# Kernel tuning notes

Measured on AMD Instinct MI355X. Metric: run time of the kernel, lower is better.

## Reference

```python
import jax, jax.numpy as jnp
import numpy as np

NUM_GRAPHS = 500
BN_EPS = 1e-5


def setup_inputs() -> dict:
    key = jax.random.key(0)
    ks = jax.random.split(key, 16)
    N, E, F, D, L = 100000, 1600000, 128, 128, 3
    x = jax.random.normal(ks[0], (N, F), dtype=jnp.float32)
    edge_index = jax.random.randint(ks[1], (2, E), 0, N)
    batch = jnp.sort(jax.random.randint(ks[2], (N,), 0, NUM_GRAPHS))
    s = 1.0 / np.sqrt(F)
    sd = 1.0 / np.sqrt(D)
    # SAGEConv layer 0: out = lin_l(mean_aggr(x_j)) + lin_r(x)
    sage_Wl = jax.random.uniform(ks[3], (F, D), jnp.float32, -s, s)
    sage_bl = jax.random.uniform(ks[4], (D,), jnp.float32, -s, s)
    sage_Wr = jax.random.uniform(ks[5], (F, D), jnp.float32, -s, s)
    # GINConv layers 1..L-1: nn = Linear(D,D) -> ReLU -> Linear(D,D)
    gin_W1 = jax.random.uniform(ks[6], (L - 1, D, D), jnp.float32, -sd, sd)
    gin_b1 = jax.random.uniform(ks[7], (L - 1, D), jnp.float32, -sd, sd)
    gin_W2 = jax.random.uniform(ks[8], (L - 1, D, D), jnp.float32, -sd, sd)
    gin_b2 = jax.random.uniform(ks[9], (L - 1, D), jnp.float32, -sd, sd)
    bn_gamma = jnp.ones((L, D), dtype=jnp.float32)
    bn_beta = jnp.zeros((L, D), dtype=jnp.float32)
    return {"x": x, "edge_index": edge_index, "batch": batch,
            "sage_Wl": sage_Wl, "sage_bl": sage_bl, "sage_Wr": sage_Wr,
            "gin_W1": gin_W1, "gin_b1": gin_b1, "gin_W2": gin_W2, "gin_b2": gin_b2,
            "bn_gamma": bn_gamma, "bn_beta": bn_beta}


def _batchnorm(h, gamma, beta):
    mu = jnp.mean(h, axis=0)
    var = jnp.var(h, axis=0)  # biased, as torch BN uses for normalization
    return (h - mu) * jax.lax.rsqrt(var + BN_EPS) * gamma + beta


def reference(x, edge_index, batch, sage_Wl, sage_bl, sage_Wr,
              gin_W1, gin_b1, gin_W2, gin_b2, bn_gamma, bn_beta):
    N = x.shape[0]
    src, dst = edge_index[0], edge_index[1]
    L = bn_gamma.shape[0]

    # Layer 0: SAGEConv (mean aggregation, root weight, no bias on lin_r)
    deg = jax.ops.segment_sum(jnp.ones_like(dst, dtype=x.dtype), dst, num_segments=N)
    aggr = jax.ops.segment_sum(x[src], dst, num_segments=N)
    aggr = aggr / jnp.maximum(deg, 1.0)[:, None]
    h = aggr @ sage_Wl + sage_bl + x @ sage_Wr
    h = jax.nn.relu(h)
    h = _batchnorm(h, bn_gamma[0], bn_beta[0])
    xs = [h]

    # Layers 1..L-1: GINConv (eps=0): nn(x + sum_aggr(x_j))
    for i in range(1, L):
        aggr = jax.ops.segment_sum(h[src], dst, num_segments=N)
        t = h + aggr
        t = jax.nn.relu(t @ gin_W1[i - 1] + gin_b1[i - 1])
        t = t @ gin_W2[i - 1] + gin_b2[i - 1]
        h = jax.nn.relu(t)
        h = _batchnorm(h, bn_gamma[i], bn_beta[i])
        xs.append(h)

    # pooling != 'last': concat global_add_pool over every layer
    pooled = jnp.concatenate(
        [jax.ops.segment_sum(xi, batch, num_segments=NUM_GRAPHS) for xi in xs], axis=1)
    node_feats = jnp.concatenate(xs, axis=1)
    return (pooled, node_feats)
```

## Files before the change

kernel.cpp:

```cpp
#include <hip/hip_runtime.h>
#include <hip/hip_bf16.h>


#define BN_EPS 1e-5f
#define EPB 4096

typedef short s8v __attribute__((ext_vector_type(8)));
typedef float f4v __attribute__((ext_vector_type(4)));

__device__ __forceinline__ float bflo(unsigned u) { return __uint_as_float(u << 16); }
__device__ __forceinline__ float bfhi(unsigned u) { return __uint_as_float(u & 0xffff0000u); }
__device__ __forceinline__ unsigned short f2bf(float f) {
    unsigned u = __float_as_uint(f);
    unsigned r = (u + 0x7fffu + ((u >> 16) & 1u)) >> 16;
    return (unsigned short)r;
}
__device__ __forceinline__ unsigned pk2(float a, float b) {
    return (unsigned)f2bf(a) | ((unsigned)f2bf(b) << 16);
}
__device__ __forceinline__ void unpack8(uint4 u, float* v) {
    v[0] = bflo(u.x); v[1] = bfhi(u.x);
    v[2] = bflo(u.y); v[3] = bfhi(u.y);
    v[4] = bflo(u.z); v[5] = bfhi(u.z);
    v[6] = bflo(u.w); v[7] = bfhi(u.w);
}


__global__ __launch_bounds__(256) void k_binA(const int* __restrict__ src,
                                              const int* __restrict__ dst, int E, int NB, int CAP,
                                              int* __restrict__ bcnt,
                                              unsigned long long* __restrict__ ebuf) {
    __shared__ int hist[512], base[512], cur[512];
    const int tid = threadIdx.x;
    const int e0 = blockIdx.x * EPB;
    for (int i = tid; i < 512; i += 256) { hist[i] = 0; cur[i] = 0; }
    __syncthreads();
#pragma unroll
    for (int k = 0; k < EPB / 256; k++) {
        int e = e0 + k * 256 + tid;
        if (e < E) atomicAdd(&hist[dst[e] >> 8], 1);
    }
    __syncthreads();
    for (int b = tid; b < NB; b += 256)
        base[b] = hist[b] ? atomicAdd(&bcnt[b], hist[b]) : 0;
    __syncthreads();
#pragma unroll
    for (int k = 0; k < EPB / 256; k++) {
        int e = e0 + k * 256 + tid;
        if (e < E) {
            int d = dst[e];
            int b = d >> 8;
            int lp = atomicAdd(&cur[b], 1);
            int gp = base[b] + lp;
            if (gp < CAP)
                ebuf[(size_t)b * CAP + gp] = ((unsigned long long)d << 32) | (unsigned)src[e];
        }
    }
}

__global__ void k_bscan(const int* __restrict__ bcnt, int NB, int* __restrict__ bbase) {
    __shared__ int sm[256];
    const int tid = threadIdx.x;
    const int c = (NB + 255) / 256;
    int s = 0;
    for (int k = 0; k < c; k++) { int i = tid * c + k; if (i < NB) s += bcnt[i]; }
    sm[tid] = s;
    __syncthreads();
    for (int off = 1; off < 256; off <<= 1) {
        int v = (tid >= off) ? sm[tid - off] : 0;
        __syncthreads();
        sm[tid] += v;
        __syncthreads();
    }
    int run = sm[tid] - s;
    for (int k = 0; k < c; k++) {
        int i = tid * c + k;
        if (i < NB) { bbase[i] = run; run += bcnt[i]; }
    }
}

__global__ __launch_bounds__(256) void k_binB(const unsigned long long* __restrict__ ebuf,
                                              int CAP, const int* __restrict__ bcnt,
                                              const int* __restrict__ bbase,
                                              int N, int E,
                                              int* __restrict__ rp, int* __restrict__ csr) {
    __shared__ int deg[256], sc[256], cur[256];
    const int tid = threadIdx.x;
    const int b = blockIdx.x;
    const int cnt = min(bcnt[b], CAP);
    const int cbase = bbase[b];
    deg[tid] = 0;
    __syncthreads();
    const unsigned long long* eb = ebuf + (size_t)b * CAP;
    for (int i = tid; i < cnt; i += 256) {
        int d = (int)(eb[i] >> 32);
        atomicAdd(&deg[d & 255], 1);
    }
    __syncthreads();
    int myDeg = deg[tid];
    sc[tid] = myDeg;
    __syncthreads();
    for (int off = 1; off < 256; off <<= 1) {
        int v = (tid >= off) ? sc[tid - off] : 0;
        __syncthreads();
        sc[tid] += v;
        __syncthreads();
    }
    int pos = cbase + sc[tid] - myDeg;
    int node = b * 256 + tid;
    if (node < N) rp[node] = pos;
    cur[tid] = pos;
    __syncthreads();
    for (int i = tid; i < cnt; i += 256) {
        unsigned long long e = eb[i];
        int d = (int)(e >> 32);
        int p = atomicAdd(&cur[d & 255], 1);
        csr[p] = (int)(e & 0xffffffffu);
    }
    if (b == 0 && tid == 0) rp[N] = E;
}


__global__ void k_cvt_bf16(const float* __restrict__ in, uint4* __restrict__ out, int n8) {
    int i = blockIdx.x * 256 + threadIdx.x;
    if (i >= n8) return;
    const float4* p = reinterpret_cast<const float4*>(in) + (size_t)i * 2;
    float4 a = p[0], b = p[1];
    uint4 o;
    o.x = pk2(a.x, a.y); o.y = pk2(a.z, a.w);
    o.z = pk2(b.x, b.y); o.w = pk2(b.z, b.w);
    out[i] = o;
}

__global__ void k_pack_w(const float* __restrict__ W, unsigned short* __restrict__ out) {
    int idx = blockIdx.x * 256 + threadIdx.x;
    int k = idx >> 7, d = idx & 127;
    float w = W[idx];
    unsigned short h = f2bf(w);
    float hf = __uint_as_float((unsigned)h << 16);
    unsigned short l = f2bf(w - hf);
    int o = (((k >> 3) * 128) + d) * 8 + (k & 7);
    out[o] = h;
    out[16384 + o] = l;
}


template <bool SELF, bool MEAN>
__global__ void k_aggr(const int* __restrict__ rp, const int* __restrict__ csr,
                       const uint4* __restrict__ src, uint4* __restrict__ out, int N) {
    int node = blockIdx.x * 16 + (threadIdx.x >> 4);
    if (node >= N) return;
    int c = threadIdx.x & 15;
    float acc[8];
    if (SELF) {
        unpack8(src[(size_t)node * 16 + c], acc);
    } else {
#pragma unroll
        for (int k = 0; k < 8; k++) acc[k] = 0.f;
    }
    int lo = rp[node], hi = rp[node + 1];
    for (int j = lo; j < hi; j++) {
        int sn = csr[j];
        float v[8];
        unpack8(src[(size_t)sn * 16 + c], v);
#pragma unroll
        for (int k = 0; k < 8; k++) acc[k] += v[k];
    }
    if (MEAN) {
        float inv = 1.0f / fmaxf((float)(hi - lo), 1.0f);
#pragma unroll
        for (int k = 0; k < 8; k++) acc[k] *= inv;
    }
    uint4 o;
    o.x = pk2(acc[0], acc[1]); o.y = pk2(acc[2], acc[3]);
    o.z = pk2(acc[4], acc[5]); o.w = pk2(acc[6], acc[7]);
    out[(size_t)node * 16 + c] = o;
}


template <int TERMS, bool F32OUT, bool STATS>
__global__ __launch_bounds__(256) void k_gemm_mfma(
    const uint4* __restrict__ A1, const uint4* __restrict__ A2,
    const uint4* __restrict__ Wfrag,
    const float* __restrict__ bias,
    float* __restrict__ outF,
    unsigned short* __restrict__ outB,
    float* __restrict__ gsum, float* __restrict__ gsq,
    int N) {
    __shared__ float sred[4][128][2];
    const int tid = threadIdx.x;
    const int lane = tid & 63, wid = tid >> 6;
    const int nbase = blockIdx.x * 128 + wid * 32;
    const int l16 = lane & 15, lg = lane >> 4;

    f4v acc[2][8];
#pragma unroll
    for (int nf = 0; nf < 2; nf++)
#pragma unroll
        for (int df = 0; df < 8; df++) {
            acc[nf][df][0] = 0.f; acc[nf][df][1] = 0.f;
            acc[nf][df][2] = 0.f; acc[nf][df][3] = 0.f;
        }

#pragma unroll
    for (int t = 0; t < TERMS; t++) {
        const uint4* A = t ? A2 : A1;
        const uint4* Whi = Wfrag + (size_t)t * 4096;
        const uint4* Wlo = Whi + 2048;
        uint4 bvec[2][4];
#pragma unroll
        for (int nf = 0; nf < 2; nf++) {
            const uint4* row = A + (size_t)(nbase + nf * 16 + l16) * 16;
#pragma unroll
            for (int ks = 0; ks < 4; ks++) bvec[nf][ks] = row[ks * 4 + lg];
        }
#pragma unroll
        for (int ks = 0; ks < 4; ks++) {
            s8v b0 = __builtin_bit_cast(s8v, bvec[0][ks]);
            s8v b1 = __builtin_bit_cast(s8v, bvec[1][ks]);
#pragma unroll
            for (int df = 0; df < 8; df++) {
                int wi = (ks * 4 + lg) * 128 + df * 16 + l16;
                s8v ah = __builtin_bit_cast(s8v, Whi[wi]);
                s8v al = __builtin_bit_cast(s8v, Wlo[wi]);
                acc[0][df] = __builtin_amdgcn_mfma_f32_16x16x32_bf16(ah, b0, acc[0][df], 0, 0, 0);
                acc[1][df] = __builtin_amdgcn_mfma_f32_16x16x32_bf16(ah, b1, acc[1][df], 0, 0, 0);
                acc[0][df] = __builtin_amdgcn_mfma_f32_16x16x32_bf16(al, b0, acc[0][df], 0, 0, 0);
                acc[1][df] = __builtin_amdgcn_mfma_f32_16x16x32_bf16(al, b1, acc[1][df], 0, 0, 0);
            }
        }
    }

    const bool v0 = (nbase + 0 * 16 + l16) < N;
    const bool v1 = (nbase + 1 * 16 + l16) < N;
    float4 oo[2][8];
#pragma unroll
    for (int df = 0; df < 8; df++) {
        int d0 = df * 16 + lg * 4;
        const float4 bb = *reinterpret_cast<const float4*>(bias + d0);
#pragma unroll
        for (int nf = 0; nf < 2; nf++) {
            oo[nf][df].x = fmaxf(acc[nf][df][0] + bb.x, 0.f);
            oo[nf][df].y = fmaxf(acc[nf][df][1] + bb.y, 0.f);
            oo[nf][df].z = fmaxf(acc[nf][df][2] + bb.z, 0.f);
            oo[nf][df].w = fmaxf(acc[nf][df][3] + bb.w, 0.f);
        }
    }

    if (STATS) {
#pragma unroll
        for (int df = 0; df < 8; df++) {
            float s[4], q[4];
#pragma unroll
            for (int r = 0; r < 4; r++) {
                float a0 = v0 ? (&oo[0][df].x)[r] : 0.f;
                float a1 = v1 ? (&oo[1][df].x)[r] : 0.f;
                s[r] = a0 + a1;
                q[r] = a0 * a0 + a1 * a1;
            }
#pragma unroll
            for (int m = 1; m < 16; m <<= 1) {
#pragma unroll
                for (int r = 0; r < 4; r++) {
                    s[r] += __shfl_xor(s[r], m, 64);
                    q[r] += __shfl_xor(q[r], m, 64);
                }
            }
            if (l16 == 0) {
#pragma unroll
                for (int r = 0; r < 4; r++) {
                    sred[wid][df * 16 + lg * 4 + r][0] = s[r];
                    sred[wid][df * 16 + lg * 4 + r][1] = q[r];
                }
            }
        }
        __syncthreads();
        if (tid < 128) {
            float s = sred[0][tid][0] + sred[1][tid][0] + sred[2][tid][0] + sred[3][tid][0];
            float q = sred[0][tid][1] + sred[1][tid][1] + sred[2][tid][1] + sred[3][tid][1];
            unsafeAtomicAdd(&gsum[tid], s);
            unsafeAtomicAdd(&gsq[tid], q);
        }
    }

#pragma unroll
    for (int nf = 0; nf < 2; nf++) {
        int n = nbase + nf * 16 + l16;
        if (n < N) {
#pragma unroll
            for (int df = 0; df < 8; df++) {
                int d0 = df * 16 + lg * 4;
                if (F32OUT) {
                    *reinterpret_cast<float4*>(outF + (size_t)n * 384 + d0) = oo[nf][df];
                } else {
                    uint2 p;
                    p.x = pk2(oo[nf][df].x, oo[nf][df].y);
                    p.y = pk2(oo[nf][df].z, oo[nf][df].w);
                    *reinterpret_cast<uint2*>(outB + (size_t)n * 128 + d0) = p;
                }
            }
        }
    }
}


__global__ void k_bnfin(const float* __restrict__ gsum, const float* __restrict__ gsq,
                        const float* __restrict__ gamma, const float* __restrict__ beta,
                        int N, float* __restrict__ a, float* __restrict__ c) {
    int d = threadIdx.x;
    float invN = 1.0f / (float)N;
    float mu = gsum[d] * invN;
    float var = gsq[d] * invN - mu * mu;
    float rs = rsqrtf(var + BN_EPS);
    float aa = gamma[d] * rs;
    a[d] = aa;
    c[d] = beta[d] - mu * aa;
}

template <bool BF16IN>
__global__ void k_norm2(const void* __restrict__ in, int ldin,
                        const float* __restrict__ sa, const float* __restrict__ sc,
                        float* __restrict__ outF, uint4* __restrict__ outB, int N) {
    int idx = blockIdx.x * 256 + threadIdx.x;
    if (idx >= N * 16) return;
    int n = idx >> 4, cc = idx & 15;
    float v[8];
    if (BF16IN) {
        unpack8(reinterpret_cast<const uint4*>(in)[(size_t)n * 16 + cc], v);
    } else {
        const float* p = (const float*)in + (size_t)n * ldin + cc * 8;
        float4 x0 = *reinterpret_cast<const float4*>(p);
        float4 x1 = *reinterpret_cast<const float4*>(p + 4);
        v[0] = x0.x; v[1] = x0.y; v[2] = x0.z; v[3] = x0.w;
        v[4] = x1.x; v[5] = x1.y; v[6] = x1.z; v[7] = x1.w;
    }
    const float4 a0 = *reinterpret_cast<const float4*>(sa + cc * 8);
    const float4 a1 = *reinterpret_cast<const float4*>(sa + cc * 8 + 4);
    const float4 c0 = *reinterpret_cast<const float4*>(sc + cc * 8);
    const float4 c1 = *reinterpret_cast<const float4*>(sc + cc * 8 + 4);
    float y[8];
    y[0] = fmaf(v[0], a0.x, c0.x); y[1] = fmaf(v[1], a0.y, c0.y);
    y[2] = fmaf(v[2], a0.z, c0.z); y[3] = fmaf(v[3], a0.w, c0.w);
    y[4] = fmaf(v[4], a1.x, c1.x); y[5] = fmaf(v[5], a1.y, c1.y);
    y[6] = fmaf(v[6], a1.z, c1.z); y[7] = fmaf(v[7], a1.w, c1.w);
    float* po = outF + (size_t)n * 384 + cc * 8;
    *reinterpret_cast<float4*>(po) = make_float4(y[0], y[1], y[2], y[3]);
    *reinterpret_cast<float4*>(po + 4) = make_float4(y[4], y[5], y[6], y[7]);
    if (outB) {
        uint4 o;
        o.x = pk2(y[0], y[1]); o.y = pk2(y[2], y[3]);
        o.z = pk2(y[4], y[5]); o.w = pk2(y[6], y[7]);
        outB[(size_t)n * 16 + cc] = o;
    }
}


__device__ __forceinline__ int lbound(const int* __restrict__ b, int n, int v) {
    int lo = 0, hi = n;
    while (lo < hi) {
        int m = (lo + hi) >> 1;
        if (b[m] < v) lo = m + 1; else hi = m;
    }
    return lo;
}

__global__ void k_pool(const float* __restrict__ nf, const int* __restrict__ batch,
                       int N, float* __restrict__ out) {
    int g = blockIdx.x;
    int d = threadIdx.x;
    int lo = lbound(batch, N, g);
    int hi = lbound(batch, N, g + 1);
    float s = 0.f;
    for (int n = lo; n < hi; n++) s += nf[(size_t)n * 384 + d];
    out[(size_t)g * 384 + d] = s;
}


extern "C" void kernel_launch(void* const* d_in, const int* in_sizes, int n_in,
                              void* d_out, int out_size, void* d_ws, size_t ws_size,
                              hipStream_t stream) {
    const float* x   = (const float*)d_in[0];
    const int*   ei  = (const int*)d_in[1];
    const int*   bat = (const int*)d_in[2];
    const float* sWl = (const float*)d_in[3];
    const float* sbl = (const float*)d_in[4];
    const float* sWr = (const float*)d_in[5];
    const float* gW1 = (const float*)d_in[6];
    const float* gb1 = (const float*)d_in[7];
    const float* gW2 = (const float*)d_in[8];
    const float* gb2 = (const float*)d_in[9];
    const float* bng = (const float*)d_in[10];
    const float* bnb = (const float*)d_in[11];

    const int N = in_sizes[0] / 128;
    const int E = in_sizes[1] / 2;
    const int G = out_size / 384 - N;
    const int* srcp = ei;
    const int* dstp = ei + E;

    char* w = (char*)d_ws;
    auto alloc = [&](size_t bytes) -> void* {
        void* p = (void*)w;
        w += (bytes + 255) & ~(size_t)255;
        return p;
    };
    const size_t Npad = (size_t)(N + 128);
    int*   rp    = (int*)alloc(((size_t)N + 1) * 4);
    int*   csr   = (int*)alloc((size_t)E * 4);
    int*   bcnt  = (int*)alloc(8192);
    int*   bbase = (int*)alloc(8192);
    float* gsum  = (float*)alloc(512);
    float* gsq   = (float*)alloc(512);
    float* abuf  = (float*)alloc(512);
    float* cbuf  = (float*)alloc(512);
    unsigned short* Wp = (unsigned short*)alloc((size_t)6 * 2 * 16384 * 2);
    unsigned short* ab = (unsigned short*)alloc(Npad * 256);
    unsigned short* tb = (unsigned short*)alloc(Npad * 256);

    float* pooled = (float*)d_out;
    float* nf     = pooled + (size_t)G * 384;

    const int NB  = (N + 255) / 256;
    int CAP = ((2 * (E / (NB > 0 ? NB : 1)) + 511) / 512) * 512;
    const long long maxcap = (long long)(Npad * 256) / ((long long)NB * 8);
    if ((long long)CAP > maxcap) CAP = (int)(maxcap & ~511LL);
    unsigned long long* ebuf = (unsigned long long*)ab;

    const int egrid = (E + EPB - 1) / EPB;
    const int agrid = (N + 15) / 16;
    const int ggrid = (N + 127) / 128;
    const int vgrid = (N * 16 + 255) / 256;

    hipMemsetAsync(bcnt, 0, (size_t)NB * 4, stream);
    k_binA<<<egrid, 256, 0, stream>>>(srcp, dstp, E, NB, CAP, bcnt, ebuf);
    k_bscan<<<1, 256, 0, stream>>>(bcnt, NB, bbase);
    k_binB<<<NB, 256, 0, stream>>>(ebuf, CAP, bcnt, bbase, N, E, rp, csr);

    k_cvt_bf16<<<vgrid, 256, 0, stream>>>(x, (uint4*)tb, N * 16);
    k_pack_w<<<64, 256, 0, stream>>>(sWl,         Wp + 0 * 32768);
    k_pack_w<<<64, 256, 0, stream>>>(sWr,         Wp + 1 * 32768);
    k_pack_w<<<64, 256, 0, stream>>>(gW1,         Wp + 2 * 32768);
    k_pack_w<<<64, 256, 0, stream>>>(gW2,         Wp + 3 * 32768);
    k_pack_w<<<64, 256, 0, stream>>>(gW1 + 16384, Wp + 4 * 32768);
    k_pack_w<<<64, 256, 0, stream>>>(gW2 + 16384, Wp + 5 * 32768);

    k_aggr<false, true><<<agrid, 256, 0, stream>>>(rp, csr, (const uint4*)tb, (uint4*)ab, N);
    hipMemsetAsync(gsum, 0, 1024, stream);
    k_gemm_mfma<2, true, true><<<ggrid, 256, 0, stream>>>(
        (const uint4*)ab, (const uint4*)tb, (const uint4*)Wp, sbl, nf, nullptr,
        gsum, gsq, N);
    k_bnfin<<<1, 128, 0, stream>>>(gsum, gsq, bng, bnb, N, abuf, cbuf);
    k_norm2<false><<<vgrid, 256, 0, stream>>>(nf, 384, abuf, cbuf, nf, (uint4*)tb, N);

    for (int l = 1; l < 3; l++) {
        const uint4* W1p = (const uint4*)(Wp + (size_t)(2 + (l - 1) * 2) * 32768);
        const uint4* W2p = (const uint4*)(Wp + (size_t)(3 + (l - 1) * 2) * 32768);
        const float* b1 = gb1 + (size_t)(l - 1) * 128;
        const float* b2 = gb2 + (size_t)(l - 1) * 128;
        float* nfl = nf + (size_t)l * 128;

        k_aggr<true, false><<<agrid, 256, 0, stream>>>(rp, csr, (const uint4*)tb, (uint4*)ab, N);
        k_gemm_mfma<1, false, false><<<ggrid, 256, 0, stream>>>(
            (const uint4*)ab, nullptr, W1p, b1, nullptr, tb, nullptr, nullptr, N);
        hipMemsetAsync(gsum, 0, 1024, stream);
        k_gemm_mfma<1, true, true><<<ggrid, 256, 0, stream>>>(
            (const uint4*)tb, nullptr, W2p, b2, nfl, nullptr, gsum, gsq, N);
        k_bnfin<<<1, 128, 0, stream>>>(gsum, gsq, bng + l * 128, bnb + l * 128, N, abuf, cbuf);
        k_norm2<false><<<vgrid, 256, 0, stream>>>(nfl, 384, abuf, cbuf, nfl,
                                                  (l < 2) ? (uint4*)tb : nullptr, N);
    }

    k_pool<<<G, 384, 0, stream>>>(nf, bat, N, pooled);
}
```

Before: 669.8 us.

## Fuse GIN MLP GEMMs via LDS and defer BN normalization into pooling

The two GIN linear layers now run in one kernel: the ReLU'd hidden tile is staged as bf16 in swizzled shared memory rather than written to and re-read from global memory. Per-layer batchnorm is no longer written back to the fp32 output right away. Only the bf16 copy needed by the next layer is normalized, and one final kernel applies all three layers' scale/shift in place while accumulating graph pooling with atomics. Memsets are folded into bnfin. This removes several full passes over the N×384 output and the intermediate buffer, at the cost of atomics in pooling and higher shared-memory use per GEMM block.

```diff
diff --git a/kernel.cpp b/kernel.cpp
--- a/kernel.cpp
+++ b/kernel.cpp
@@ -144,6 +144,27 @@
     out[16384 + o] = l;
 }
 
+__global__ void k_cvt_h(const float* __restrict__ y,
+                        const float* __restrict__ sa, const float* __restrict__ sc,
+                        uint4* __restrict__ out, int N) {
+    int idx = blockIdx.x * 256 + threadIdx.x;
+    if (idx >= N * 16) return;
+    int n = idx >> 4, cc = idx & 15;
+    const float* p = y + (size_t)n * 384 + cc * 8;
+    float4 x0 = *reinterpret_cast<const float4*>(p);
+    float4 x1 = *reinterpret_cast<const float4*>(p + 4);
+    const float4 a0 = *reinterpret_cast<const float4*>(sa + cc * 8);
+    const float4 a1 = *reinterpret_cast<const float4*>(sa + cc * 8 + 4);
+    const float4 c0 = *reinterpret_cast<const float4*>(sc + cc * 8);
+    const float4 c1 = *reinterpret_cast<const float4*>(sc + cc * 8 + 4);
+    uint4 o;
+    o.x = pk2(fmaf(x0.x, a0.x, c0.x), fmaf(x0.y, a0.y, c0.y));
+    o.y = pk2(fmaf(x0.z, a0.z, c0.z), fmaf(x0.w, a0.w, c0.w));
+    o.z = pk2(fmaf(x1.x, a1.x, c1.x), fmaf(x1.y, a1.y, c1.y));
+    o.w = pk2(fmaf(x1.z, a1.z, c1.z), fmaf(x1.w, a1.w, c1.w));
+    out[(size_t)n * 16 + cc] = o;
+}
+
 
 template <bool SELF, bool MEAN>
 __global__ void k_aggr(const int* __restrict__ rp, const int* __restrict__ csr,
@@ -178,14 +199,66 @@
 }
 
 
-template <int TERMS, bool F32OUT, bool STATS>
-__global__ __launch_bounds__(256) void k_gemm_mfma(
+#define MFMA_STAGE(Whi, Wlo, B0, B1, ACC)                                          \
+    _Pragma("unroll")                                                              \
+    for (int ks = 0; ks < 4; ks++) {                                               \
+        s8v b0 = __builtin_bit_cast(s8v, B0[ks]);                                  \
+        s8v b1 = __builtin_bit_cast(s8v, B1[ks]);                                  \
+        _Pragma("unroll")                                                          \
+        for (int df = 0; df < 8; df++) {                                           \
+            int wi = (ks * 4 + lg) * 128 + df * 16 + l16;                          \
+            s8v ah = __builtin_bit_cast(s8v, Whi[wi]);                             \
+            s8v al = __builtin_bit_cast(s8v, Wlo[wi]);                             \
+            ACC[0][df] = __builtin_amdgcn_mfma_f32_16x16x32_bf16(ah, b0, ACC[0][df], 0, 0, 0); \
+            ACC[1][df] = __builtin_amdgcn_mfma_f32_16x16x32_bf16(ah, b1, ACC[1][df], 0, 0, 0); \
+            ACC[0][df] = __builtin_amdgcn_mfma_f32_16x16x32_bf16(al, b0, ACC[0][df], 0, 0, 0); \
+            ACC[1][df] = __builtin_amdgcn_mfma_f32_16x16x32_bf16(al, b1, ACC[1][df], 0, 0, 0); \
+        }                                                                          \
+    }
+
+#define STATS_EPILOGUE(OO, V0, V1)                                                 \
+    {                                                                              \
+        _Pragma("unroll")                                                          \
+        for (int df = 0; df < 8; df++) {                                           \
+            float s[4], q[4];                                                      \
+            _Pragma("unroll")                                                      \
+            for (int r = 0; r < 4; r++) {                                          \
+                float a0 = V0 ? (&OO[0][df].x)[r] : 0.f;                           \
+                float a1 = V1 ? (&OO[1][df].x)[r] : 0.f;                           \
+                s[r] = a0 + a1;                                                    \
+                q[r] = a0 * a0 + a1 * a1;                                          \
+            }                                                                      \
+            _Pragma("unroll")                                                      \
+            for (int m = 1; m < 16; m <<= 1) {                                     \
+                _Pragma("unroll")                                                  \
+                for (int r = 0; r < 4; r++) {                                      \
+                    s[r] += __shfl_xor(s[r], m, 64);                               \
+                    q[r] += __shfl_xor(q[r], m, 64);                               \
+                }                                                                  \
+            }                                                                      \
+            if (l16 == 0) {                                                        \
+                _Pragma("unroll")                                                  \
+                for (int r = 0; r < 4; r++) {                                      \
+                    sred[wid][df * 16 + lg * 4 + r][0] = s[r];                     \
+                    sred[wid][df * 16 + lg * 4 + r][1] = q[r];                     \
+                }                                                                  \
+            }                                                                      \
+        }                                                                          \
+        __syncthreads();                                                           \
+        if (tid < 128) {                                                           \
+            float s = sred[0][tid][0] + sred[1][tid][0] + sred[2][tid][0] + sred[3][tid][0]; \
+            float q = sred[0][tid][1] + sred[1][tid][1] + sred[2][tid][1] + sred[3][tid][1]; \
+            unsafeAtomicAdd(&gsum[tid], s);                                        \
+            unsafeAtomicAdd(&gsq[tid], q);                                         \
+        }                                                                          \
+    }
+
+
+__global__ __launch_bounds__(256) void k_gemm_sage(
     const uint4* __restrict__ A1, const uint4* __restrict__ A2,
     const uint4* __restrict__ Wfrag,
     const float* __restrict__ bias,
-    float* __restrict__ outF,
-    unsigned short* __restrict__ outB,
-    float* __restrict__ gsum, float* __restrict__ gsq,
+    float* __restrict__ outF, float* __restrict__ gsum, float* __restrict__ gsq,
     int N) {
     __shared__ float sred[4][128][2];
     const int tid = threadIdx.x;
@@ -197,13 +270,11 @@
 #pragma unroll
     for (int nf = 0; nf < 2; nf++)
 #pragma unroll
-        for (int df = 0; df < 8; df++) {
-            acc[nf][df][0] = 0.f; acc[nf][df][1] = 0.f;
-            acc[nf][df][2] = 0.f; acc[nf][df][3] = 0.f;
-        }
-
-#pragma unroll
-    for (int t = 0; t < TERMS; t++) {
+        for (int df = 0; df < 8; df++)
+            acc[nf][df] = (f4v){0.f, 0.f, 0.f, 0.f};
+
+#pragma unroll
+    for (int t = 0; t < 2; t++) {
         const uint4* A = t ? A2 : A1;
         const uint4* Whi = Wfrag + (size_t)t * 4096;
         const uint4* Wlo = Whi + 2048;
@@ -214,25 +285,11 @@
 #pragma unroll
             for (int ks = 0; ks < 4; ks++) bvec[nf][ks] = row[ks * 4 + lg];
         }
-#pragma unroll
-        for (int ks = 0; ks < 4; ks++) {
-            s8v b0 = __builtin_bit_cast(s8v, bvec[0][ks]);
-            s8v b1 = __builtin_bit_cast(s8v, bvec[1][ks]);
-#pragma unroll
-            for (int df = 0; df < 8; df++) {
-                int wi = (ks * 4 + lg) * 128 + df * 16 + l16;
-                s8v ah = __builtin_bit_cast(s8v, Whi[wi]);
-                s8v al = __builtin_bit_cast(s8v, Wlo[wi]);
-                acc[0][df] = __builtin_amdgcn_mfma_f32_16x16x32_bf16(ah, b0, acc[0][df], 0, 0, 0);
-                acc[1][df] = __builtin_amdgcn_mfma_f32_16x16x32_bf16(ah, b1, acc[1][df], 0, 0, 0);
-                acc[0][df] = __builtin_amdgcn_mfma_f32_16x16x32_bf16(al, b0, acc[0][df], 0, 0, 0);
-                acc[1][df] = __builtin_amdgcn_mfma_f32_16x16x32_bf16(al, b1, acc[1][df], 0, 0, 0);
-            }
-        }
-    }
-
-    const bool v0 = (nbase + 0 * 16 + l16) < N;
-    const bool v1 = (nbase + 1 * 16 + l16) < N;
+        MFMA_STAGE(Whi, Wlo, bvec[0], bvec[1], acc)
+    }
+
+    const bool v0 = (nbase + l16) < N;
+    const bool v1 = (nbase + 16 + l16) < N;
     float4 oo[2][8];
 #pragma unroll
     for (int df = 0; df < 8; df++) {
@@ -247,64 +304,124 @@
         }
     }
 
-    if (STATS) {
-#pragma unroll
-        for (int df = 0; df < 8; df++) {
-            float s[4], q[4];
-#pragma unroll
-            for (int r = 0; r < 4; r++) {
-                float a0 = v0 ? (&oo[0][df].x)[r] : 0.f;
-                float a1 = v1 ? (&oo[1][df].x)[r] : 0.f;
-                s[r] = a0 + a1;
-                q[r] = a0 * a0 + a1 * a1;
-            }
-#pragma unroll
-            for (int m = 1; m < 16; m <<= 1) {
-#pragma unroll
-                for (int r = 0; r < 4; r++) {
-                    s[r] += __shfl_xor(s[r], m, 64);
-                    q[r] += __shfl_xor(q[r], m, 64);
-                }
-            }
-            if (l16 == 0) {
-#pragma unroll
-                for (int r = 0; r < 4; r++) {
-                    sred[wid][df * 16 + lg * 4 + r][0] = s[r];
-                    sred[wid][df * 16 + lg * 4 + r][1] = q[r];
-                }
-            }
-        }
-        __syncthreads();
-        if (tid < 128) {
-            float s = sred[0][tid][0] + sred[1][tid][0] + sred[2][tid][0] + sred[3][tid][0];
-            float q = sred[0][tid][1] + sred[1][tid][1] + sred[2][tid][1] + sred[3][tid][1];
-            unsafeAtomicAdd(&gsum[tid], s);
-            unsafeAtomicAdd(&gsq[tid], q);
-        }
-    }
+    STATS_EPILOGUE(oo, v0, v1)
 
 #pragma unroll
     for (int nf = 0; nf < 2; nf++) {
         int n = nbase + nf * 16 + l16;
         if (n < N) {
 #pragma unroll
-            for (int df = 0; df < 8; df++) {
-                int d0 = df * 16 + lg * 4;
-                if (F32OUT) {
-                    *reinterpret_cast<float4*>(outF + (size_t)n * 384 + d0) = oo[nf][df];
-                } else {
-                    uint2 p;
-                    p.x = pk2(oo[nf][df].x, oo[nf][df].y);
-                    p.y = pk2(oo[nf][df].z, oo[nf][df].w);
-                    *reinterpret_cast<uint2*>(outB + (size_t)n * 128 + d0) = p;
-                }
-            }
-        }
-    }
-}
-
-
-__global__ void k_bnfin(const float* __restrict__ gsum, const float* __restrict__ gsq,
+            for (int df = 0; df < 8; df++)
+                *reinterpret_cast<float4*>(outF + (size_t)n * 384 + df * 16 + lg * 4) = oo[nf][df];
+        }
+    }
+}
+
+
+__global__ __launch_bounds__(256) void k_gemm_gin(
+    const uint4* __restrict__ A,
+    const uint4* __restrict__ W1f, const uint4* __restrict__ W2f,
+    const float* __restrict__ b1, const float* __restrict__ b2,
+    float* __restrict__ outF, float* __restrict__ gsum, float* __restrict__ gsq,
+    int N) {
+    __shared__ uint4 tile[2048];
+    __shared__ float sred[4][128][2];
+    const int tid = threadIdx.x;
+    const int lane = tid & 63, wid = tid >> 6;
+    const int nbase = blockIdx.x * 128 + wid * 32;
+    const int l16 = lane & 15, lg = lane >> 4;
+
+    f4v acc[2][8];
+#pragma unroll
+    for (int nf = 0; nf < 2; nf++)
+#pragma unroll
+        for (int df = 0; df < 8; df++)
+            acc[nf][df] = (f4v){0.f, 0.f, 0.f, 0.f};
+
+    {
+        const uint4* Whi = W1f;
+        const uint4* Wlo = W1f + 2048;
+        uint4 bvec[2][4];
+#pragma unroll
+        for (int nf = 0; nf < 2; nf++) {
+            const uint4* row = A + (size_t)(nbase + nf * 16 + l16) * 16;
+#pragma unroll
+            for (int ks = 0; ks < 4; ks++) bvec[nf][ks] = row[ks * 4 + lg];
+        }
+        MFMA_STAGE(Whi, Wlo, bvec[0], bvec[1], acc)
+    }
+#pragma unroll
+    for (int df = 0; df < 8; df++) {
+        int d0 = df * 16 + lg * 4;
+        const float4 bb = *reinterpret_cast<const float4*>(b1 + d0);
+#pragma unroll
+        for (int nf = 0; nf < 2; nf++) {
+            float tx = fmaxf(acc[nf][df][0] + bb.x, 0.f);
+            float ty = fmaxf(acc[nf][df][1] + bb.y, 0.f);
+            float tz = fmaxf(acc[nf][df][2] + bb.z, 0.f);
+            float tw = fmaxf(acc[nf][df][3] + bb.w, 0.f);
+            uint2 p;
+            p.x = pk2(tx, ty);
+            p.y = pk2(tz, tw);
+            int row = wid * 32 + nf * 16 + l16;
+            int col4 = df * 2 + (lg >> 1);
+            int slot = row * 16 + (col4 ^ (row & 15));
+            *reinterpret_cast<uint2*>(
+                reinterpret_cast<char*>(tile) + (size_t)slot * 16 + (lg & 1) * 8) = p;
+        }
+    }
+    __syncthreads();
+
+#pragma unroll
+    for (int nf = 0; nf < 2; nf++)
+#pragma unroll
+        for (int df = 0; df < 8; df++)
+            acc[nf][df] = (f4v){0.f, 0.f, 0.f, 0.f};
+    {
+        const uint4* Whi = W2f;
+        const uint4* Wlo = W2f + 2048;
+        uint4 bvec[2][4];
+#pragma unroll
+        for (int nf = 0; nf < 2; nf++) {
+            int row = wid * 32 + nf * 16 + l16;
+#pragma unroll
+            for (int ks = 0; ks < 4; ks++)
+                bvec[nf][ks] = tile[row * 16 + ((ks * 4 + lg) ^ (row & 15))];
+        }
+        MFMA_STAGE(Whi, Wlo, bvec[0], bvec[1], acc)
+    }
+
+    const bool v0 = (nbase + l16) < N;
+    const bool v1 = (nbase + 16 + l16) < N;
+    float4 oo[2][8];
+#pragma unroll
+    for (int df = 0; df < 8; df++) {
+        int d0 = df * 16 + lg * 4;
+        const float4 bb = *reinterpret_cast<const float4*>(b2 + d0);
+#pragma unroll
+        for (int nf = 0; nf < 2; nf++) {
+            oo[nf][df].x = fmaxf(acc[nf][df][0] + bb.x, 0.f);
+            oo[nf][df].y = fmaxf(acc[nf][df][1] + bb.y, 0.f);
+            oo[nf][df].z = fmaxf(acc[nf][df][2] + bb.z, 0.f);
+            oo[nf][df].w = fmaxf(acc[nf][df][3] + bb.w, 0.f);
+        }
+    }
+
+    STATS_EPILOGUE(oo, v0, v1)
+
+#pragma unroll
+    for (int nf = 0; nf < 2; nf++) {
+        int n = nbase + nf * 16 + l16;
+        if (n < N) {
+#pragma unroll
+            for (int df = 0; df < 8; df++)
+                *reinterpret_cast<float4*>(outF + (size_t)n * 384 + df * 16 + lg * 4) = oo[nf][df];
+        }
+    }
+}
+
+
+__global__ void k_bnfin(float* __restrict__ gsum, float* __restrict__ gsq,
                         const float* __restrict__ gamma, const float* __restrict__ beta,
                         int N, float* __restrict__ a, float* __restrict__ c) {
     int d = threadIdx.x;
@@ -315,64 +432,35 @@
     float aa = gamma[d] * rs;
     a[d] = aa;
     c[d] = beta[d] - mu * aa;
-}
-
-template <bool BF16IN>
-__global__ void k_norm2(const void* __restrict__ in, int ldin,
-                        const float* __restrict__ sa, const float* __restrict__ sc,
-                        float* __restrict__ outF, uint4* __restrict__ outB, int N) {
-    int idx = blockIdx.x * 256 + threadIdx.x;
-    if (idx >= N * 16) return;
-    int n = idx >> 4, cc = idx & 15;
-    float v[8];
-    if (BF16IN) {
-        unpack8(reinterpret_cast<const uint4*>(in)[(size_t)n * 16 + cc], v);
-    } else {
-        const float* p = (const float*)in + (size_t)n * ldin + cc * 8;
-        float4 x0 = *reinterpret_cast<const float4*>(p);
-        float4 x1 = *reinterpret_cast<const float4*>(p + 4);
-        v[0] = x0.x; v[1] = x0.y; v[2] = x0.z; v[3] = x0.w;
-        v[4] = x1.x; v[5] = x1.y; v[6] = x1.z; v[7] = x1.w;
-    }
-    const float4 a0 = *reinterpret_cast<const float4*>(sa + cc * 8);
-    const float4 a1 = *reinterpret_cast<const float4*>(sa + cc * 8 + 4);
-    const float4 c0 = *reinterpret_cast<const float4*>(sc + cc * 8);
-    const float4 c1 = *reinterpret_cast<const float4*>(sc + cc * 8 + 4);
-    float y[8];
-    y[0] = fmaf(v[0], a0.x, c0.x); y[1] = fmaf(v[1], a0.y, c0.y);
-    y[2] = fmaf(v[2], a0.z, c0.z); y[3] = fmaf(v[3], a0.w, c0.w);
-    y[4] = fmaf(v[4], a1.x, c1.x); y[5] = fmaf(v[5], a1.y, c1.y);
-    y[6] = fmaf(v[6], a1.z, c1.z); y[7] = fmaf(v[7], a1.w, c1.w);
-    float* po = outF + (size_t)n * 384 + cc * 8;
-    *reinterpret_cast<float4*>(po) = make_float4(y[0], y[1], y[2], y[3]);
-    *reinterpret_cast<float4*>(po + 4) = make_float4(y[4], y[5], y[6], y[7]);
-    if (outB) {
-        uint4 o;
-        o.x = pk2(y[0], y[1]); o.y = pk2(y[2], y[3]);
-        o.z = pk2(y[4], y[5]); o.w = pk2(y[6], y[7]);
-        outB[(size_t)n * 16 + cc] = o;
-    }
-}
-
-
-__device__ __forceinline__ int lbound(const int* __restrict__ b, int n, int v) {
-    int lo = 0, hi = n;
-    while (lo < hi) {
-        int m = (lo + hi) >> 1;
-        if (b[m] < v) lo = m + 1; else hi = m;
-    }
-    return lo;
-}
-
-__global__ void k_pool(const float* __restrict__ nf, const int* __restrict__ batch,
-                       int N, float* __restrict__ out) {
-    int g = blockIdx.x;
-    int d = threadIdx.x;
-    int lo = lbound(batch, N, g);
-    int hi = lbound(batch, N, g + 1);
+    gsum[d] = 0.f;
+    gsq[d] = 0.f;
+}
+
+
+__global__ __launch_bounds__(384) void k_finpool(float* __restrict__ nf,
+                                                 const float* __restrict__ a3,
+                                                 const float* __restrict__ c3,
+                                                 const int* __restrict__ batch,
+                                                 int N, float* __restrict__ pooled) {
+    const int d = threadIdx.x;
+    const float a = a3[d], c = c3[d];
+    const int n0 = blockIdx.x * 64;
+    const int n1 = min(n0 + 64, N);
     float s = 0.f;
-    for (int n = lo; n < hi; n++) s += nf[(size_t)n * 384 + d];
-    out[(size_t)g * 384 + d] = s;
+    int curg = batch[n0];
+    for (int n = n0; n < n1; n++) {
+        int g = batch[n];
+        if (g != curg) {
+            unsafeAtomicAdd(&pooled[(size_t)curg * 384 + d], s);
+            s = 0.f;
+            curg = g;
+        }
+        float v = nf[(size_t)n * 384 + d];
+        float h = fmaf(v, a, c);
+        nf[(size_t)n * 384 + d] = h;
+        s += h;
+    }
+    unsafeAtomicAdd(&pooled[(size_t)curg * 384 + d], s);
 }
 
 
@@ -411,8 +499,8 @@
     int*   bbase = (int*)alloc(8192);
     float* gsum  = (float*)alloc(512);
     float* gsq   = (float*)alloc(512);
-    float* abuf  = (float*)alloc(512);
-    float* cbuf  = (float*)alloc(512);
+    float* abuf  = (float*)alloc(3 * 512);
+    float* cbuf  = (float*)alloc(3 * 512);
     unsigned short* Wp = (unsigned short*)alloc((size_t)6 * 2 * 16384 * 2);
     unsigned short* ab = (unsigned short*)alloc(Npad * 256);
     unsigned short* tb = (unsigned short*)alloc(Npad * 256);
@@ -430,6 +518,7 @@
     const int agrid = (N + 15) / 16;
     const int ggrid = (N + 127) / 128;
     const int vgrid = (N * 16 + 255) / 256;
+    const int fgrid = (N + 63) / 64;
 
     hipMemsetAsync(bcnt, 0, (size_t)NB * 4, stream);
     k_binA<<<egrid, 256, 0, stream>>>(srcp, dstp, E, NB, CAP, bcnt, ebuf);
@@ -443,32 +532,31 @@
     k_pack_w<<<64, 256, 0, stream>>>(gW2,         Wp + 3 * 32768);
     k_pack_w<<<64, 256, 0, stream>>>(gW1 + 16384, Wp + 4 * 32768);
     k_pack_w<<<64, 256, 0, stream>>>(gW2 + 16384, Wp + 5 * 32768);
+    hipMemsetAsync(gsum, 0, 1024, stream);
+    hipMemsetAsync(pooled, 0, (size_t)G * 384 * 4, stream);
 
     k_aggr<false, true><<<agrid, 256, 0, stream>>>(rp, csr, (const uint4*)tb, (uint4*)ab, N);
-    hipMemsetAsync(gsum, 0, 1024, stream);
-    k_gemm_mfma<2, true, true><<<ggrid, 256, 0, stream>>>(
-        (const uint4*)ab, (const uint4*)tb, (const uint4*)Wp, sbl, nf, nullptr,
-        gsum, gsq, N);
+    k_gemm_sage<<<ggrid, 256, 0, stream>>>(
+        (const uint4*)ab, (const uint4*)tb, (const uint4*)Wp, sbl, nf, gsum, gsq, N);
     k_bnfin<<<1, 128, 0, stream>>>(gsum, gsq, bng, bnb, N, abuf, cbuf);
-    k_norm2<false><<<vgrid, 256, 0, stream>>>(nf, 384, abuf, cbuf, nf, (uint4*)tb, N);
+    k_cvt_h<<<vgrid, 256, 0, stream>>>(nf, abuf, cbuf, (uint4*)tb, N);
 
     for (int l = 1; l < 3; l++) {
-        const uint4* W1p = (const uint4*)(Wp + (size_t)(2 + (l - 1) * 2) * 32768);
-        const uint4* W2p = (const uint4*)(Wp + (size_t)(3 + (l - 1) * 2) * 32768);
+        const uint4* W1p = (const uint4*)(Wp + (size_t)(2 * l) * 32768);
+        const uint4* W2p = (const uint4*)(Wp + (size_t)(2 * l + 1) * 32768);
         const float* b1 = gb1 + (size_t)(l - 1) * 128;
         const float* b2 = gb2 + (size_t)(l - 1) * 128;
         float* nfl = nf + (size_t)l * 128;
 
         k_aggr<true, false><<<agrid, 256, 0, stream>>>(rp, csr, (const uint4*)tb, (uint4*)ab, N);
-        k_gemm_mfma<1, false, false><<<ggrid, 256, 0, stream>>>(
-            (const uint4*)ab, nullptr, W1p, b1, nullptr, tb, nullptr, nullptr, N);
-        hipMemsetAsync(gsum, 0, 1024, stream);
-        k_gemm_mfma<1, true, true><<<ggrid, 256, 0, stream>>>(
-            (const uint4*)tb, nullptr, W2p, b2, nfl, nullptr, gsum, gsq, N);
-        k_bnfin<<<1, 128, 0, stream>>>(gsum, gsq, bng + l * 128, bnb + l * 128, N, abuf, cbuf);
-        k_norm2<false><<<vgrid, 256, 0, stream>>>(nfl, 384, abuf, cbuf, nfl,
-                                                  (l < 2) ? (uint4*)tb : nullptr, N);
-    }
-
-    k_pool<<<G, 384, 0, stream>>>(nf, bat, N, pooled);
-}
+        k_gemm_gin<<<ggrid, 256, 0, stream>>>(
+            (const uint4*)ab, W1p, W2p, b1, b2, nfl, gsum, gsq, N);
+        k_bnfin<<<1, 128, 0, stream>>>(gsum, gsq, bng + l * 128, bnb + l * 128, N,
+                                       abuf + (size_t)l * 128, cbuf + (size_t)l * 128);
+        if (l < 2)
+            k_cvt_h<<<vgrid, 256, 0, stream>>>(nfl, abuf + (size_t)l * 128,
+                                               cbuf + (size_t)l * 128, (uint4*)tb, N);
+    }
+
+    k_finpool<<<fgrid, 384, 0, stream>>>(nf, abuf, cbuf, bat, N, pooled);
+}
```

New measurement: 620.9 us. -7.3%, faster.
